# Performance work log

Measured on AMD Instinct MI355X. Metric: run time of the kernel, lower is better.

Reference implementation:

```python
import jax, jax.numpy as jnp
import numpy as np
import heapq

N = 256          # num nodes (also num start-node runs)
T = 5 * N        # message budget per run (graph.num_nodes * 5)
IN = 128         # in_features
H = 256          # hidden
M = 128          # message_size
OUT = 64         # out_features
E = 768          # directed edge list length (undirected adjacency built from it)


def _build_schedule(edge_index, n, t_max, rng):
    """Deterministically replay the heap simulation from the torch module.
    Returns proc[n,T] (node popped at each step), parent[n,T] (index of the
    step whose output message is consumed; -1 => first_message), valid[n,T]."""
    adj = [set() for _ in range(n)]
    src, dst = edge_index
    for s, d in zip(src, dst):
        adj[int(s)].add(int(d))
        adj[int(d)].add(int(s))
    adj = [sorted(a) for a in adj]
    proc = np.zeros((n, t_max), np.int32)
    parent = np.full((n, t_max), -1, np.int32)
    valid = np.zeros((n, t_max), bool)
    for i in range(n):
        heap = [(0.0, 0, i, -1)]  # (delay, tiebreak, node, parent_step)
        cnt = 1
        t = 0
        while heap and t < t_max:
            delay, _, node, par = heapq.heappop(heap)
            proc[i, t] = node
            parent[i, t] = par
            valid[i, t] = True
            for nb in adj[node]:
                nd = max(1e-10, rng.normal(0.5, 0.5))
                heapq.heappush(heap, (delay + nd, cnt, nb, t))
                cnt += 1
            t += 1
    return proc, parent, valid


def setup_inputs() -> dict:
    key = jax.random.key(0)
    ks = jax.random.split(key, 12)
    rng = np.random.default_rng(0)
    edge_index = rng.integers(0, N, size=(2, E))
    proc, parent, valid = _build_schedule(edge_index, N, T, rng)
    s = 0.05
    return {
        "x": jax.random.normal(ks[0], (N, IN), jnp.float32),
        "first_message": jnp.zeros((1, M), jnp.float32),
        "We": jax.random.normal(ks[1], (H, IN), jnp.float32) * s,
        "be": jax.random.normal(ks[2], (H,), jnp.float32) * s,
        "Ws": jax.random.normal(ks[3], (H, H + M), jnp.float32) * s,
        "bs": jax.random.normal(ks[4], (H,), jnp.float32) * s,
        "Wm": jax.random.normal(ks[5], (M, H + M), jnp.float32) * s,
        "bm": jax.random.normal(ks[6], (M,), jnp.float32) * s,
        "Wd": jax.random.normal(ks[7], (OUT, H), jnp.float32) * s,
        "bd": jax.random.normal(ks[8], (OUT,), jnp.float32) * s,
        "proc": jnp.asarray(proc),
        "parent": jnp.asarray(parent),
        "valid": jnp.asarray(valid),
    }


def reference(x, first_message, We, be, Ws, bs, Wm, bm, Wd, bd, proc, parent, valid):
    n = x.shape[0]
    t_max = proc.shape[1]
    m = first_message.shape[1]
    pred0 = x @ We.T + be  # encoder, recomputed fresh for every run -> shared [N,H]
    fmsg = first_message[0]

    def run(proc_i, parent_i, valid_i):
        msgs0 = jnp.zeros((t_max, m), x.dtype)

        def step(carry, inp):
            pred, msgs = carry
            t, node, par, v = inp
            msg = jnp.where(par < 0, fmsg, msgs[jnp.maximum(par, 0)])
            ns = jax.nn.relu(Ws @ jnp.concatenate([pred[node], msg]) + bs)
            nm = Wm @ jnp.concatenate([ns, msg]) + bm
            pred = pred.at[node].set(jnp.where(v, ns, pred[node]))
            msgs = msgs.at[t].set(jnp.where(v, nm, msgs[t]))
            return (pred, msgs), None

        (pred, _), _ = jax.lax.scan(
            step, (pred0, msgs0), (jnp.arange(t_max), proc_i, parent_i, valid_i)
        )
        return pred

    preds = jax.vmap(run)(proc, parent, valid)  # [N, N, H]
    diag = preds[jnp.arange(n), jnp.arange(n)]  # node i's state after run started at i
    return jax.nn.log_softmax(diag @ Wd.T + bd, axis=-1)  # [N, OUT]
```

## Files before the change

### kernel.cpp

```cpp
#include <hip/hip_runtime.h>
#include <stdint.h>

typedef _Float16 half_t;
typedef _Float16 half2_t __attribute__((ext_vector_type(2)));

#define NN   256
#define TT   1280
#define INF  128
#define HH   256
#define MM   128
#define OUTF 64
#define HM   384

#define THREADS 512

#define LDS_PRED    0
#define LDS_PROC    131072
#define LDS_PARENT  136192
#define LDS_FMSG    141312
#define LDS_V2      141568
#define SMEM_BYTES  143104

#define WS_PRED0    0
#define WS_WSH      131072
#define WS_WMH      327680
#define WS_MSGS     425984

__device__ __forceinline__ float dot2f(half2_t a, half2_t b, float c) {
#if __has_builtin(__builtin_amdgcn_fdot2)
  return __builtin_amdgcn_fdot2(a, b, c, false);
#else
  return c + (float)a[0] * (float)b[0] + (float)a[1] * (float)b[1];
#endif
}

template <int CTRL>
__device__ __forceinline__ float dpp_add(float x) {
  int xi = __float_as_int(x);
  int yi = __builtin_amdgcn_update_dpp(xi, xi, CTRL, 0xf, 0xf, false);
  return x + __int_as_float(yi);
}
__device__ __forceinline__ float row16_reduce(float x) {
  x = dpp_add<0xB1>(x);
  x = dpp_add<0x4E>(x);
  x = dpp_add<0x141>(x);
  x = dpp_add<0x140>(x);
  return x;
}

__global__ __launch_bounds__(256)
void prep_kernel(const float* __restrict__ Ws, const float* __restrict__ Wm,
                 half_t* __restrict__ WsH, half_t* __restrict__ WmH)
{
  const int i = blockIdx.x * 256 + threadIdx.x;
  if (i < HH * HM) WsH[i] = (half_t)Ws[i];
  else             WmH[i - HH * HM] = (half_t)Wm[i - HH * HM];
}

__global__ __launch_bounds__(256)
void enc_kernel(const float* __restrict__ x, const float* __restrict__ We,
                const float* __restrict__ be, half_t* __restrict__ pred0)
{
  __shared__ float xs[INF];
  const int n = blockIdx.x;
  const int hh = threadIdx.x;
  if (hh < INF) xs[hh] = x[n * INF + hh];
  __syncthreads();
  const float* w = We + hh * INF;
  float acc = be[hh];
#pragma unroll 16
  for (int k = 0; k < INF; ++k) acc += w[k] * xs[k];
  pred0[n * HH + hh] = (half_t)acc;
}

__global__ __launch_bounds__(THREADS, 2)
void sim_kernel(const half_t* __restrict__ WsH, const float* __restrict__ bs,
                const half_t* __restrict__ WmH, const float* __restrict__ bm,
                const float* __restrict__ Wd, const float* __restrict__ bd,
                const float* __restrict__ fmsg,
                const int* __restrict__ proc, const int* __restrict__ parent,
                const half_t* __restrict__ pred0,
                half_t* __restrict__ msgs,
                float* __restrict__ out)
{
  extern __shared__ char smem[];
  half_t* lds_pred        = (half_t*)(smem + LDS_PRED);
  int* lds_proc           = (int*)(smem + LDS_PROC);
  int* lds_par            = (int*)(smem + LDS_PARENT);
  half_t* lds_fmsg        = (half_t*)(smem + LDS_FMSG);
  char* v2base            = smem + LDS_V2;

  const int tid  = threadIdx.x;
  const int run  = blockIdx.x;
  const int wave = tid >> 6;
  const int lane = tid & 63;
  const int c    = lane & 15;
  const int rg   = wave * 4 + (lane >> 4);
  const int obyte = c * 48;

  int w1i[96];
  {
    const char* wb = (const char*)WsH + (size_t)(rg * 8) * (HM * 2) + obyte;
#pragma unroll
    for (int r = 0; r < 8; ++r)
#pragma unroll
      for (int jj = 0; jj < 3; ++jj) {
        int4 v = *(const int4*)(wb + r * (HM * 2) + jj * 16);
        w1i[r * 12 + jj * 4 + 0] = v.x;
        w1i[r * 12 + jj * 4 + 1] = v.y;
        w1i[r * 12 + jj * 4 + 2] = v.z;
        w1i[r * 12 + jj * 4 + 3] = v.w;
      }
  }
  int w2i[48];
  {
    const char* wb = (const char*)WmH + (size_t)(rg * 4) * (HM * 2) + obyte;
#pragma unroll
    for (int r = 0; r < 4; ++r)
#pragma unroll
      for (int jj = 0; jj < 3; ++jj) {
        int4 v = *(const int4*)(wb + r * (HM * 2) + jj * 16);
        w2i[r * 12 + jj * 4 + 0] = v.x;
        w2i[r * 12 + jj * 4 + 1] = v.y;
        w2i[r * 12 + jj * 4 + 2] = v.z;
        w2i[r * 12 + jj * 4 + 3] = v.w;
      }
  }
#pragma unroll
  for (int j = 0; j < 96; ++j) asm volatile("" : "+v"(w1i[j]));
#pragma unroll
  for (int j = 0; j < 48; ++j) asm volatile("" : "+v"(w2i[j]));

  const float bs1 = (c < 8) ? bs[rg * 8 + c] : 0.f;
  const float bm1 = (c < 4) ? bm[rg * 4 + c] : 0.f;

  {
    const uint4* s = (const uint4*)pred0;
    uint4* d = (uint4*)lds_pred;
#pragma unroll
    for (int i = 0; i < (NN * HH * 2 / 16) / THREADS; ++i)
      d[tid + i * THREADS] = s[tid + i * THREADS];
  }
  {
    const int* procR = proc + run * TT;
    const int* parR  = parent + run * TT;
    for (int i = tid; i < TT; i += THREADS) {
      lds_proc[i] = procR[i];
      lds_par[i]  = parR[i];
    }
  }
  if (tid < MM) lds_fmsg[tid] = (half_t)fmsg[tid];
  __syncthreads();

  half_t* msgs_run = msgs + (size_t)run * TT * MM;

  {
    const int p0 = lds_par[0];
    if (tid < 16) {
      uint4 v;
      if (p0 < 0) v = *(const uint4*)((const char*)lds_fmsg + tid * 16);
      else        v = *(const uint4*)((const char*)(msgs_run + (size_t)p0 * MM) + tid * 16);
      *(uint4*)(v2base + 512 + tid * 16) = v;
    }
  }
  __syncthreads();

  uint4 pfB = make_uint4(0, 0, 0, 0);

  int b = 0;
  for (int t = 0; t < TT; ++t, b ^= 1) {
    const int node  = lds_proc[t];
    const int vld   = (t == 0) | (lds_par[t] >= 0);
    const int parn1 = (t + 1 < TT) ? lds_par[t + 1] : -1;
    const int parn2 = (t + 2 < TT) ? lds_par[t + 2] : -1;

    const bool useA = (parn1 >= 0) && (parn1 == t - 1);
    uint4 pfA;
    if (tid < 16 && useA)
      pfA = *(const uint4*)((const char*)(msgs_run + (size_t)parn1 * MM) + tid * 16);

    const char* predrow = (const char*)(lds_pred + node * HH);
    const char* msgb    = v2base + b * 768 + 512;
    int av[12];
    {
#pragma unroll
      for (int j = 0; j < 3; ++j) {
        const int o = obyte + j * 16;
        const char* p = (o < 512) ? (predrow + o) : (msgb + (o - 512));
        int4 A = *(const int4*)p;
        av[j * 4 + 0] = A.x; av[j * 4 + 1] = A.y;
        av[j * 4 + 2] = A.z; av[j * 4 + 3] = A.w;
      }
    }
    float acc0 = 0.f, acc1 = 0.f, acc2_ = 0.f, acc3 = 0.f;
    float acc4 = 0.f, acc5 = 0.f, acc6 = 0.f, acc7 = 0.f;
#pragma unroll
    for (int k = 0; k < 12; ++k) {
      const half2_t a = __builtin_bit_cast(half2_t, av[k]);
      acc0 = dot2f(a, __builtin_bit_cast(half2_t, w1i[0 * 12 + k]), acc0);
      acc1 = dot2f(a, __builtin_bit_cast(half2_t, w1i[1 * 12 + k]), acc1);
      acc2_ = dot2f(a, __builtin_bit_cast(half2_t, w1i[2 * 12 + k]), acc2_);
      acc3 = dot2f(a, __builtin_bit_cast(half2_t, w1i[3 * 12 + k]), acc3);
      acc4 = dot2f(a, __builtin_bit_cast(half2_t, w1i[4 * 12 + k]), acc4);
      acc5 = dot2f(a, __builtin_bit_cast(half2_t, w1i[5 * 12 + k]), acc5);
      acc6 = dot2f(a, __builtin_bit_cast(half2_t, w1i[6 * 12 + k]), acc6);
      acc7 = dot2f(a, __builtin_bit_cast(half2_t, w1i[7 * 12 + k]), acc7);
    }
    float nsv = 0.f;
    {
      float s;
      s = row16_reduce(acc0); if (c == 0) nsv = s;
      s = row16_reduce(acc1); if (c == 1) nsv = s;
      s = row16_reduce(acc2_); if (c == 2) nsv = s;
      s = row16_reduce(acc3); if (c == 3) nsv = s;
      s = row16_reduce(acc4); if (c == 4) nsv = s;
      s = row16_reduce(acc5); if (c == 5) nsv = s;
      s = row16_reduce(acc6); if (c == 6) nsv = s;
      s = row16_reduce(acc7); if (c == 7) nsv = s;
    }
    nsv = fmaxf(nsv + bs1, 0.f);
    const half_t nsh = (half_t)nsv;
    if (c < 8) ((half_t*)(v2base + b * 768))[rg * 8 + c] = nsh;

    if (t + 1 < TT && tid < 16) {
      char* dst = v2base + (b ^ 1) * 768 + 512 + tid * 16;
      if (parn1 < 0)
        *(uint4*)dst = *(const uint4*)((const char*)lds_fmsg + tid * 16);
      else if (parn1 != t)
        *(uint4*)dst = useA ? pfA : pfB;
    }
    if (tid < 16 && parn2 >= 0 && parn2 < t)
      pfB = *(const uint4*)((const char*)(msgs_run + (size_t)parn2 * MM) + tid * 16);

    __syncthreads();

    const char* v2b = v2base + b * 768;
    int bv[12];
    {
#pragma unroll
      for (int j = 0; j < 3; ++j) {
        int4 B = *(const int4*)(v2b + obyte + j * 16);
        bv[j * 4 + 0] = B.x; bv[j * 4 + 1] = B.y;
        bv[j * 4 + 2] = B.z; bv[j * 4 + 3] = B.w;
      }
    }
    float m0 = 0.f, m1 = 0.f, m2 = 0.f, m3 = 0.f;
#pragma unroll
    for (int k = 0; k < 12; ++k) {
      const half2_t a = __builtin_bit_cast(half2_t, bv[k]);
      m0 = dot2f(a, __builtin_bit_cast(half2_t, w2i[0 * 12 + k]), m0);
      m1 = dot2f(a, __builtin_bit_cast(half2_t, w2i[1 * 12 + k]), m1);
      m2 = dot2f(a, __builtin_bit_cast(half2_t, w2i[2 * 12 + k]), m2);
      m3 = dot2f(a, __builtin_bit_cast(half2_t, w2i[3 * 12 + k]), m3);
    }
    float nmv = 0.f;
    {
      float s;
      s = row16_reduce(m0); if (c == 0) nmv = s;
      s = row16_reduce(m1); if (c == 1) nmv = s;
      s = row16_reduce(m2); if (c == 2) nmv = s;
      s = row16_reduce(m3); if (c == 3) nmv = s;
    }
    if (c < 4) {
      nmv += bm1;
      const half_t nmh = vld ? (half_t)nmv : (half_t)0.f;
      const int row2 = rg * 4 + c;
      if (vld) msgs_run[(size_t)t * MM + row2] = nmh;
      if (parn1 == t)
        ((half_t*)(v2base + (b ^ 1) * 768 + 512))[row2] = nmh;
    }
    if (c < 8 && vld)
      lds_pred[node * HH + rg * 8 + c] = nsh;
    __syncthreads();
  }

  if (tid < OUTF) {
    const float* wd = Wd + tid * HH;
    float acc = bd[tid];
#pragma unroll 8
    for (int k = 0; k < HH; ++k) acc += wd[k] * (float)lds_pred[run * HH + k];
    float m = acc;
#pragma unroll
    for (int off = 32; off >= 1; off >>= 1) m = fmaxf(m, __shfl_xor(m, off));
    const float e = __expf(acc - m);
    float s = e;
#pragma unroll
    for (int off = 32; off >= 1; off >>= 1) s += __shfl_xor(s, off);
    out[run * OUTF + tid] = acc - m - logf(s);
  }
}

extern "C" void kernel_launch(void* const* d_in, const int* in_sizes, int n_in,
                              void* d_out, int out_size, void* d_ws, size_t ws_size,
                              hipStream_t stream) {
  (void)in_sizes; (void)n_in; (void)out_size; (void)ws_size;
  const float* x    = (const float*)d_in[0];
  const float* fm   = (const float*)d_in[1];
  const float* We   = (const float*)d_in[2];
  const float* be   = (const float*)d_in[3];
  const float* Ws   = (const float*)d_in[4];
  const float* bs   = (const float*)d_in[5];
  const float* Wm   = (const float*)d_in[6];
  const float* bm   = (const float*)d_in[7];
  const float* Wd   = (const float*)d_in[8];
  const float* bd   = (const float*)d_in[9];
  const int* proc   = (const int*)d_in[10];
  const int* parent = (const int*)d_in[11];
  float* out = (float*)d_out;

  half_t* pred0 = (half_t*)((char*)d_ws + WS_PRED0);
  half_t* WsH   = (half_t*)((char*)d_ws + WS_WSH);
  half_t* WmH   = (half_t*)((char*)d_ws + WS_WMH);
  half_t* msgs  = (half_t*)((char*)d_ws + WS_MSGS);

  (void)hipFuncSetAttribute((const void*)sim_kernel,
                            hipFuncAttributeMaxDynamicSharedMemorySize, SMEM_BYTES);

  prep_kernel<<<dim3((HH * HM + MM * HM) / 256), dim3(256), 0, stream>>>(Ws, Wm, WsH, WmH);
  enc_kernel<<<dim3(NN), dim3(256), 0, stream>>>(x, We, be, pred0);
  sim_kernel<<<dim3(NN), dim3(THREADS), SMEM_BYTES, stream>>>(
      WsH, bs, WmH, bm, Wd, bd, fm, proc, parent, pred0, msgs, out);
}
```

Before: 2.003 ms.

## Double threads per run block and restructure cross-lane reductions with transpose-style DPP/swizzle

Raises the sim block from 512 to 1024 threads so each thread owns half as many weight columns (32 lanes per row group instead of 16), halving per-thread register weights and dot work per step. Rewrites the reductions so partial sums are first reduced within quads, then selected per lane and finished with row-shift DPP and a ds_swizzle, avoiding eight full independent row reductions. Drops the two-step-ahead prefetch of parent messages, keeping only a one-step-ahead global load. Higher thread count per block changes occupancy and adds swizzle latency, and the shallower prefetch may expose global load latency.

```diff
diff --git a/kernel.cpp b/kernel.cpp
--- a/kernel.cpp
+++ b/kernel.cpp
@@ -12,7 +12,7 @@
 #define OUTF 64
 #define HM   384
 
-#define THREADS 512
+#define THREADS 1024
 
 #define LDS_PRED    0
 #define LDS_PROC    131072
@@ -40,12 +40,9 @@
   int yi = __builtin_amdgcn_update_dpp(xi, xi, CTRL, 0xf, 0xf, false);
   return x + __int_as_float(yi);
 }
-__device__ __forceinline__ float row16_reduce(float x) {
-  x = dpp_add<0xB1>(x);
-  x = dpp_add<0x4E>(x);
-  x = dpp_add<0x141>(x);
-  x = dpp_add<0x140>(x);
-  return x;
+__device__ __forceinline__ float swz16_add(float x) {
+  int r = __builtin_amdgcn_ds_swizzle(__float_as_int(x), 0x401F);
+  return x + __int_as_float(r);
 }
 
 __global__ __launch_bounds__(256)
@@ -73,7 +70,8 @@
   pred0[n * HH + hh] = (half_t)acc;
 }
 
-__global__ __launch_bounds__(THREADS, 2)
+__global__ __attribute__((amdgpu_flat_work_group_size(THREADS, THREADS),
+                          amdgpu_waves_per_eu(4, 4)))
 void sim_kernel(const half_t* __restrict__ WsH, const float* __restrict__ bs,
                 const half_t* __restrict__ WmH, const float* __restrict__ bm,
                 const float* __restrict__ Wd, const float* __restrict__ bd,
@@ -92,47 +90,41 @@
 
   const int tid  = threadIdx.x;
   const int run  = blockIdx.x;
-  const int wave = tid >> 6;
-  const int lane = tid & 63;
-  const int c    = lane & 15;
-  const int rg   = wave * 4 + (lane >> 4);
-  const int obyte = c * 48;
-
-  int w1i[96];
+  const int rg   = tid >> 5;
+  const int c    = tid & 31;
+  const int obyte = c * 24;
+
+  int w1i[48];
   {
     const char* wb = (const char*)WsH + (size_t)(rg * 8) * (HM * 2) + obyte;
 #pragma unroll
     for (int r = 0; r < 8; ++r)
 #pragma unroll
       for (int jj = 0; jj < 3; ++jj) {
-        int4 v = *(const int4*)(wb + r * (HM * 2) + jj * 16);
-        w1i[r * 12 + jj * 4 + 0] = v.x;
-        w1i[r * 12 + jj * 4 + 1] = v.y;
-        w1i[r * 12 + jj * 4 + 2] = v.z;
-        w1i[r * 12 + jj * 4 + 3] = v.w;
+        int2 v = *(const int2*)(wb + r * (HM * 2) + jj * 8);
+        w1i[r * 6 + jj * 2 + 0] = v.x;
+        w1i[r * 6 + jj * 2 + 1] = v.y;
       }
   }
-  int w2i[48];
+  int w2i[24];
   {
     const char* wb = (const char*)WmH + (size_t)(rg * 4) * (HM * 2) + obyte;
 #pragma unroll
     for (int r = 0; r < 4; ++r)
 #pragma unroll
       for (int jj = 0; jj < 3; ++jj) {
-        int4 v = *(const int4*)(wb + r * (HM * 2) + jj * 16);
-        w2i[r * 12 + jj * 4 + 0] = v.x;
-        w2i[r * 12 + jj * 4 + 1] = v.y;
-        w2i[r * 12 + jj * 4 + 2] = v.z;
-        w2i[r * 12 + jj * 4 + 3] = v.w;
+        int2 v = *(const int2*)(wb + r * (HM * 2) + jj * 8);
+        w2i[r * 6 + jj * 2 + 0] = v.x;
+        w2i[r * 6 + jj * 2 + 1] = v.y;
       }
   }
 #pragma unroll
-  for (int j = 0; j < 96; ++j) asm volatile("" : "+v"(w1i[j]));
-#pragma unroll
-  for (int j = 0; j < 48; ++j) asm volatile("" : "+v"(w2i[j]));
-
-  const float bs1 = (c < 8) ? bs[rg * 8 + c] : 0.f;
-  const float bm1 = (c < 4) ? bm[rg * 4 + c] : 0.f;
+  for (int j = 0; j < 48; ++j) asm volatile("" : "+v"(w1i[j]));
+#pragma unroll
+  for (int j = 0; j < 24; ++j) asm volatile("" : "+v"(w2i[j]));
+
+  const float bs1 = bs[rg * 8 + (c & 7)];
+  const float bm1 = bm[rg * 4 + (c & 3)];
 
   {
     const uint4* s = (const uint4*)pred0;
@@ -165,60 +157,58 @@
   }
   __syncthreads();
 
-  uint4 pfB = make_uint4(0, 0, 0, 0);
-
   int b = 0;
   for (int t = 0; t < TT; ++t, b ^= 1) {
     const int node  = lds_proc[t];
     const int vld   = (t == 0) | (lds_par[t] >= 0);
     const int parn1 = (t + 1 < TT) ? lds_par[t + 1] : -1;
-    const int parn2 = (t + 2 < TT) ? lds_par[t + 2] : -1;
-
-    const bool useA = (parn1 >= 0) && (parn1 == t - 1);
+
     uint4 pfA;
-    if (tid < 16 && useA)
+    if (tid < 16 && parn1 >= 0 && parn1 < t)
       pfA = *(const uint4*)((const char*)(msgs_run + (size_t)parn1 * MM) + tid * 16);
 
     const char* predrow = (const char*)(lds_pred + node * HH);
     const char* msgb    = v2base + b * 768 + 512;
-    int av[12];
+    int av[6];
     {
 #pragma unroll
       for (int j = 0; j < 3; ++j) {
-        const int o = obyte + j * 16;
+        const int o = obyte + j * 8;
         const char* p = (o < 512) ? (predrow + o) : (msgb + (o - 512));
-        int4 A = *(const int4*)p;
-        av[j * 4 + 0] = A.x; av[j * 4 + 1] = A.y;
-        av[j * 4 + 2] = A.z; av[j * 4 + 3] = A.w;
+        int2 A = *(const int2*)p;
+        av[j * 2 + 0] = A.x; av[j * 2 + 1] = A.y;
       }
     }
-    float acc0 = 0.f, acc1 = 0.f, acc2_ = 0.f, acc3 = 0.f;
-    float acc4 = 0.f, acc5 = 0.f, acc6 = 0.f, acc7 = 0.f;
-#pragma unroll
-    for (int k = 0; k < 12; ++k) {
+    float acc[8];
+#pragma unroll
+    for (int r = 0; r < 8; ++r) acc[r] = 0.f;
+#pragma unroll
+    for (int k = 0; k < 6; ++k) {
       const half2_t a = __builtin_bit_cast(half2_t, av[k]);
-      acc0 = dot2f(a, __builtin_bit_cast(half2_t, w1i[0 * 12 + k]), acc0);
-      acc1 = dot2f(a, __builtin_bit_cast(half2_t, w1i[1 * 12 + k]), acc1);
-      acc2_ = dot2f(a, __builtin_bit_cast(half2_t, w1i[2 * 12 + k]), acc2_);
-      acc3 = dot2f(a, __builtin_bit_cast(half2_t, w1i[3 * 12 + k]), acc3);
-      acc4 = dot2f(a, __builtin_bit_cast(half2_t, w1i[4 * 12 + k]), acc4);
-      acc5 = dot2f(a, __builtin_bit_cast(half2_t, w1i[5 * 12 + k]), acc5);
-      acc6 = dot2f(a, __builtin_bit_cast(half2_t, w1i[6 * 12 + k]), acc6);
-      acc7 = dot2f(a, __builtin_bit_cast(half2_t, w1i[7 * 12 + k]), acc7);
-    }
-    float nsv = 0.f;
+#pragma unroll
+      for (int r = 0; r < 8; ++r)
+        acc[r] = dot2f(a, __builtin_bit_cast(half2_t, w1i[r * 6 + k]), acc[r]);
+    }
+#pragma unroll
+    for (int r = 0; r < 8; ++r) {
+      acc[r] = dpp_add<0xB1>(acc[r]);
+      acc[r] = dpp_add<0x4E>(acc[r]);
+      acc[r] = dpp_add<0x141>(acc[r]);
+    }
+    float nsv;
     {
-      float s;
-      s = row16_reduce(acc0); if (c == 0) nsv = s;
-      s = row16_reduce(acc1); if (c == 1) nsv = s;
-      s = row16_reduce(acc2_); if (c == 2) nsv = s;
-      s = row16_reduce(acc3); if (c == 3) nsv = s;
-      s = row16_reduce(acc4); if (c == 4) nsv = s;
-      s = row16_reduce(acc5); if (c == 5) nsv = s;
-      s = row16_reduce(acc6); if (c == 6) nsv = s;
-      s = row16_reduce(acc7); if (c == 7) nsv = s;
-    }
-    nsv = fmaxf(nsv + bs1, 0.f);
+      const int s = c & 7;
+      float va = (s & 1) ? acc[1] : acc[0];
+      float vb = (s & 1) ? acc[3] : acc[2];
+      float vc = (s & 1) ? acc[5] : acc[4];
+      float vd = (s & 1) ? acc[7] : acc[6];
+      float ve = (s & 2) ? vb : va;
+      float vf = (s & 2) ? vd : vc;
+      float v  = (s & 4) ? vf : ve;
+      v = dpp_add<0x128>(v);
+      v = swz16_add(v);
+      nsv = fmaxf(v + bs1, 0.f);
+    }
     const half_t nsh = (half_t)nsv;
     if (c < 8) ((half_t*)(v2base + b * 768))[rg * 8 + c] = nsh;
 
@@ -227,42 +217,46 @@
       if (parn1 < 0)
         *(uint4*)dst = *(const uint4*)((const char*)lds_fmsg + tid * 16);
       else if (parn1 != t)
-        *(uint4*)dst = useA ? pfA : pfB;
-    }
-    if (tid < 16 && parn2 >= 0 && parn2 < t)
-      pfB = *(const uint4*)((const char*)(msgs_run + (size_t)parn2 * MM) + tid * 16);
-
+        *(uint4*)dst = pfA;
+    }
     __syncthreads();
 
     const char* v2b = v2base + b * 768;
-    int bv[12];
+    int bv[6];
     {
 #pragma unroll
       for (int j = 0; j < 3; ++j) {
-        int4 B = *(const int4*)(v2b + obyte + j * 16);
-        bv[j * 4 + 0] = B.x; bv[j * 4 + 1] = B.y;
-        bv[j * 4 + 2] = B.z; bv[j * 4 + 3] = B.w;
+        int2 B = *(const int2*)(v2b + obyte + j * 8);
+        bv[j * 2 + 0] = B.x; bv[j * 2 + 1] = B.y;
       }
     }
-    float m0 = 0.f, m1 = 0.f, m2 = 0.f, m3 = 0.f;
-#pragma unroll
-    for (int k = 0; k < 12; ++k) {
+    float macc[4];
+#pragma unroll
+    for (int r = 0; r < 4; ++r) macc[r] = 0.f;
+#pragma unroll
+    for (int k = 0; k < 6; ++k) {
       const half2_t a = __builtin_bit_cast(half2_t, bv[k]);
-      m0 = dot2f(a, __builtin_bit_cast(half2_t, w2i[0 * 12 + k]), m0);
-      m1 = dot2f(a, __builtin_bit_cast(half2_t, w2i[1 * 12 + k]), m1);
-      m2 = dot2f(a, __builtin_bit_cast(half2_t, w2i[2 * 12 + k]), m2);
-      m3 = dot2f(a, __builtin_bit_cast(half2_t, w2i[3 * 12 + k]), m3);
-    }
-    float nmv = 0.f;
+#pragma unroll
+      for (int r = 0; r < 4; ++r)
+        macc[r] = dot2f(a, __builtin_bit_cast(half2_t, w2i[r * 6 + k]), macc[r]);
+    }
+#pragma unroll
+    for (int r = 0; r < 4; ++r) {
+      macc[r] = dpp_add<0xB1>(macc[r]);
+      macc[r] = dpp_add<0x4E>(macc[r]);
+    }
+    float nmv;
     {
-      float s;
-      s = row16_reduce(m0); if (c == 0) nmv = s;
-      s = row16_reduce(m1); if (c == 1) nmv = s;
-      s = row16_reduce(m2); if (c == 2) nmv = s;
-      s = row16_reduce(m3); if (c == 3) nmv = s;
+      const int s = c & 3;
+      float va = (s & 1) ? macc[1] : macc[0];
+      float vb = (s & 1) ? macc[3] : macc[2];
+      float v  = (s & 2) ? vb : va;
+      v = dpp_add<0x124>(v);
+      v = dpp_add<0x128>(v);
+      v = swz16_add(v);
+      nmv = v + bm1;
     }
     if (c < 4) {
-      nmv += bm1;
       const half_t nmh = vld ? (half_t)nmv : (half_t)0.f;
       const int row2 = rg * 4 + c;
       if (vld) msgs_run[(size_t)t * MM + row2] = nmh;
```

After: 2.424 ms. +21.1%, slower.

## Simplify message prefetch and use inline-asm dot2 with explicit waves-per-EU

Applied to the files above, without the earlier changes.

Replaces the two-stage message prefetch (pfA for parent t-1, pfB issued two steps ahead) with a single prefetch at the top of each step for any earlier parent. It also swaps the fdot2 builtin for inline v_dot2_f32_f16 asm and drops the empty asm barriers that pinned the weight registers. Launch bounds become explicit flat-work-group-size and waves-per-EU attributes, and the bias loads become unconditional masked loads. The aim is lower register pressure and a simpler loop. The cost is that the global message load is no longer hidden a step ahead, so it can sit on the per-step critical path.

```diff
diff --git a/kernel.cpp b/kernel.cpp
--- a/kernel.cpp
+++ b/kernel.cpp
@@ -26,12 +26,8 @@
 #define WS_WMH      327680
 #define WS_MSGS     425984
 
-__device__ __forceinline__ float dot2f(half2_t a, half2_t b, float c) {
-#if __has_builtin(__builtin_amdgcn_fdot2)
-  return __builtin_amdgcn_fdot2(a, b, c, false);
-#else
-  return c + (float)a[0] * (float)b[0] + (float)a[1] * (float)b[1];
-#endif
+__device__ __forceinline__ void dot2_asm(float& acc, int a, int w) {
+  asm("v_dot2_f32_f16 %0, %1, %2, %0" : "+v"(acc) : "v"(a), "v"(w));
 }
 
 template <int CTRL>
@@ -73,7 +69,8 @@
   pred0[n * HH + hh] = (half_t)acc;
 }
 
-__global__ __launch_bounds__(THREADS, 2)
+__global__ __attribute__((amdgpu_flat_work_group_size(THREADS, THREADS),
+                          amdgpu_waves_per_eu(2, 2)))
 void sim_kernel(const half_t* __restrict__ WsH, const float* __restrict__ bs,
                 const half_t* __restrict__ WmH, const float* __restrict__ bm,
                 const float* __restrict__ Wd, const float* __restrict__ bd,
@@ -126,13 +123,9 @@
         w2i[r * 12 + jj * 4 + 3] = v.w;
       }
   }
-#pragma unroll
-  for (int j = 0; j < 96; ++j) asm volatile("" : "+v"(w1i[j]));
-#pragma unroll
-  for (int j = 0; j < 48; ++j) asm volatile("" : "+v"(w2i[j]));
-
-  const float bs1 = (c < 8) ? bs[rg * 8 + c] : 0.f;
-  const float bm1 = (c < 4) ? bm[rg * 4 + c] : 0.f;
+
+  const float bs1 = bs[rg * 8 + (c & 7)];
+  const float bm1 = bm[rg * 4 + (c & 3)];
 
   {
     const uint4* s = (const uint4*)pred0;
@@ -165,18 +158,14 @@
   }
   __syncthreads();
 
-  uint4 pfB = make_uint4(0, 0, 0, 0);
-
   int b = 0;
   for (int t = 0; t < TT; ++t, b ^= 1) {
     const int node  = lds_proc[t];
     const int vld   = (t == 0) | (lds_par[t] >= 0);
     const int parn1 = (t + 1 < TT) ? lds_par[t + 1] : -1;
-    const int parn2 = (t + 2 < TT) ? lds_par[t + 2] : -1;
-
-    const bool useA = (parn1 >= 0) && (parn1 == t - 1);
+
     uint4 pfA;
-    if (tid < 16 && useA)
+    if (tid < 16 && parn1 >= 0 && parn1 < t)
       pfA = *(const uint4*)((const char*)(msgs_run + (size_t)parn1 * MM) + tid * 16);
 
     const char* predrow = (const char*)(lds_pred + node * HH);
@@ -196,15 +185,15 @@
     float acc4 = 0.f, acc5 = 0.f, acc6 = 0.f, acc7 = 0.f;
 #pragma unroll
     for (int k = 0; k < 12; ++k) {
-      const half2_t a = __builtin_bit_cast(half2_t, av[k]);
-      acc0 = dot2f(a, __builtin_bit_cast(half2_t, w1i[0 * 12 + k]), acc0);
-      acc1 = dot2f(a, __builtin_bit_cast(half2_t, w1i[1 * 12 + k]), acc1);
-      acc2_ = dot2f(a, __builtin_bit_cast(half2_t, w1i[2 * 12 + k]), acc2_);
-      acc3 = dot2f(a, __builtin_bit_cast(half2_t, w1i[3 * 12 + k]), acc3);
-      acc4 = dot2f(a, __builtin_bit_cast(half2_t, w1i[4 * 12 + k]), acc4);
-      acc5 = dot2f(a, __builtin_bit_cast(half2_t, w1i[5 * 12 + k]), acc5);
-      acc6 = dot2f(a, __builtin_bit_cast(half2_t, w1i[6 * 12 + k]), acc6);
-      acc7 = dot2f(a, __builtin_bit_cast(half2_t, w1i[7 * 12 + k]), acc7);
+      const int a = av[k];
+      dot2_asm(acc0, a, w1i[0 * 12 + k]);
+      dot2_asm(acc1, a, w1i[1 * 12 + k]);
+      dot2_asm(acc2_, a, w1i[2 * 12 + k]);
+      dot2_asm(acc3, a, w1i[3 * 12 + k]);
+      dot2_asm(acc4, a, w1i[4 * 12 + k]);
+      dot2_asm(acc5, a, w1i[5 * 12 + k]);
+      dot2_asm(acc6, a, w1i[6 * 12 + k]);
+      dot2_asm(acc7, a, w1i[7 * 12 + k]);
     }
     float nsv = 0.f;
     {
@@ -227,11 +216,8 @@
       if (parn1 < 0)
         *(uint4*)dst = *(const uint4*)((const char*)lds_fmsg + tid * 16);
       else if (parn1 != t)
-        *(uint4*)dst = useA ? pfA : pfB;
-    }
-    if (tid < 16 && parn2 >= 0 && parn2 < t)
-      pfB = *(const uint4*)((const char*)(msgs_run + (size_t)parn2 * MM) + tid * 16);
-
+        *(uint4*)dst = pfA;
+    }
     __syncthreads();
 
     const char* v2b = v2base + b * 768;
@@ -247,11 +233,11 @@
     float m0 = 0.f, m1 = 0.f, m2 = 0.f, m3 = 0.f;
 #pragma unroll
     for (int k = 0; k < 12; ++k) {
-      const half2_t a = __builtin_bit_cast(half2_t, bv[k]);
-      m0 = dot2f(a, __builtin_bit_cast(half2_t, w2i[0 * 12 + k]), m0);
-      m1 = dot2f(a, __builtin_bit_cast(half2_t, w2i[1 * 12 + k]), m1);
-      m2 = dot2f(a, __builtin_bit_cast(half2_t, w2i[2 * 12 + k]), m2);
-      m3 = dot2f(a, __builtin_bit_cast(half2_t, w2i[3 * 12 + k]), m3);
+      const int a = bv[k];
+      dot2_asm(m0, a, w2i[0 * 12 + k]);
+      dot2_asm(m1, a, w2i[1 * 12 + k]);
+      dot2_asm(m2, a, w2i[2 * 12 + k]);
+      dot2_asm(m3, a, w2i[3 * 12 + k]);
     }
     float nmv = 0.f;
     {
```

Result: slower. 2.066 ms (+3.2%).
